# Kernel tuning notes

Measured on AMD Instinct MI355X. Metric: run time of the kernel, lower is better.

The kernel has to match this reference:

```python
import jax, jax.numpy as jnp
import numpy as np

NUM_SEM, MAXPP, FS, FG, H, ITERS, ETN, GROUPS = 24, 10, 128, 128, 128, 2, 4, 16
N_NODES, N_EDGES = 20000, 320000


def _leaky(x):
    return jax.nn.leaky_relu(x, 0.01)


def _lin_init(k, din, dout):
    kw, kb = jax.random.split(k)
    lim = 1.0 / np.sqrt(din)
    w = jax.random.uniform(kw, (dout, din), jnp.float32, -lim, lim)
    b = jax.random.uniform(kb, (dout,), jnp.float32, -lim, lim)
    return w, b


def setup_inputs() -> dict:
    key = jax.random.key(0)
    ks = jax.random.split(key, 16)
    inp = {}
    inp["child_feats"] = jax.random.normal(ks[0], (1, N_NODES, NUM_SEM + MAXPP + FS), jnp.float32)
    inp["child_geo_feats"] = jax.random.normal(ks[1], (1, N_NODES, FG), jnp.float32)
    inp["child_exists"] = jnp.ones((1, N_NODES, 1), jnp.float32)
    inp["edge_type_onehot"] = jax.random.uniform(ks[2], (1, N_EDGES, ETN), jnp.float32)
    inp["edge_indices"] = jax.random.randint(ks[3], (1, N_EDGES, 2), 0, N_NODES)
    inp["child_op_w"], inp["child_op_b"] = _lin_init(ks[4], NUM_SEM + MAXPP + FS, H)
    inp["second_w"], inp["second_b"] = _lin_init(ks[5], H * (ITERS + 1), FS)
    ew, eb = zip(*[_lin_init(ks[6 + i], 2 * H + ETN, H) for i in range(ITERS)])
    inp["edge_w"] = jnp.stack(ew)
    inp["edge_b"] = jnp.stack(eb)
    inp["child_geo_w"], inp["child_geo_b"] = _lin_init(ks[10], FG, H)
    inp["second_geo_w"], inp["second_geo_b"] = _lin_init(ks[11], H, FG)
    inp["gn_w"] = jnp.ones((FG,), jnp.float32)
    inp["gn_b"] = jnp.zeros((FG,), jnp.float32)
    inp["skip_w"], inp["skip_b"] = _lin_init(ks[12], FG, FG)
    return inp


def _group_norm(x, w, b, groups=GROUPS, eps=1e-5):
    # x: [B, C]  (torch GroupNorm on 2D input)
    B, C = x.shape
    xg = x.reshape(B, groups, C // groups)
    mu = xg.mean(axis=-1, keepdims=True)
    var = xg.var(axis=-1, keepdims=True)
    xn = ((xg - mu) * jax.lax.rsqrt(var + eps)).reshape(B, C)
    return xn * w + b


def reference(child_feats, child_geo_feats, child_exists, edge_type_onehot, edge_indices,
              child_op_w, child_op_b, second_w, second_b, edge_w, edge_b,
              child_geo_w, child_geo_b, second_geo_w, second_geo_b, gn_w, gn_b, skip_w, skip_b):
    B, N, _ = child_feats.shape
    # struct branch
    cf = (child_feats @ child_op_w.T + child_op_b) * child_exists  # [B,N,H]
    iter_parent_feats = [cf.max(axis=1)]                           # symmetric_type='max'
    idx_from = edge_indices[0, :, 0]
    idx_to = edge_indices[0, :, 1]
    ef = edge_type_onehot[0]                                       # [E,ETN]
    for i in range(ITERS):
        # gather endpoints, concat edge type, edge-MLP + leaky relu
        msg = jnp.concatenate([cf[0, idx_from], cf[0, idx_to], ef], axis=1)  # [E,2H+ETN]
        msg = _leaky(msg @ edge_w[i].T + edge_b[i])                          # [E,H]
        # scatter_max into zero-initialized node slots (matches torch_scatter with out=zeros)
        cf = jnp.zeros((N, H), msg.dtype).at[idx_from].max(msg)[None]        # [1,N,H]
        iter_parent_feats.append(cf.max(axis=1))
    parent_feat = _leaky(jnp.concatenate(iter_parent_feats, axis=1) @ second_w.T + second_b)
    # geo branch
    skip = (child_geo_feats @ skip_w.T + skip_b) * child_exists    # [B,N,FG]
    cg = (child_geo_feats @ child_geo_w.T + child_geo_b) * child_exists  # [B,N,H]
    pg = _leaky(cg.max(axis=1))
    sg = _leaky(skip.max(axis=1))
    parent_geo_feat = _leaky(sg + _group_norm(pg @ second_geo_w.T + second_geo_b, gn_w, gn_b))
    return parent_feat, parent_geo_feat
```

## Files before the change

### kernel.cpp

```cpp
#include <hip/hip_runtime.h>

#define N_NODES 20000
#define N_EDGES 320000
#define HD 128
#define FIN 162
#define KE 260
#define KPAD 288
#define KOP 192
#define OSTR 200
#define GSTR 136
#define TSTR 136
#define YSTR 136
#define MAXD 64

typedef unsigned short u16;
typedef __attribute__((ext_vector_type(8))) short bf16x8;
typedef __attribute__((ext_vector_type(4))) float f32x4;

__device__ __forceinline__ float leaky(float x){ return fmaxf(x, 0.01f*x); }
__device__ __forceinline__ unsigned fmap(float f){
    unsigned u = __float_as_uint(f);
    return (u & 0x80000000u) ? ~u : (u | 0x80000000u);
}
__device__ __forceinline__ float funmap(unsigned u){
    return __uint_as_float((u & 0x80000000u) ? (u & 0x7fffffffu) : ~u);
}
__device__ __forceinline__ unsigned umax_(unsigned a, unsigned b){ return a > b ? a : b; }
__device__ __forceinline__ u16 f2bf(float x){
    unsigned b = __float_as_uint(x);
    return (u16)((b + 0x7fffu + ((b >> 16) & 1u)) >> 16);
}
__device__ __forceinline__ float bf2f(u16 u){
    return __uint_as_float(((unsigned)u) << 16);
}
__device__ __forceinline__ unsigned cvt_pk_bf16(float lo, float hi){
    unsigned r;
    asm("v_cvt_pk_bf16_f32 %0, %1, %2" : "=v"(r) : "v"(lo), "v"(hi));
    return r;
}

#define PB_W 16
#define PB_F 960
#define PB_G 640
#define PB_H 320
#define PREP_GRID (PB_W + PB_F + PB_G + PB_H)

__global__ __launch_bounds__(256) void prep(
    const float* __restrict__ edge_w, const float* __restrict__ edge_bias,
    u16* __restrict__ Wb,
    const float* __restrict__ op_w,   u16* __restrict__ Wop,
    const float* __restrict__ geo_w,  u16* __restrict__ Wgeo,
    const float* __restrict__ skip_w, u16* __restrict__ Wskip,
    const float* __restrict__ feats,  u16* __restrict__ featsb,
    const float* __restrict__ geof,   u16* __restrict__ geob,
    const int* __restrict__ eidx, const float* __restrict__ ef,
    int* __restrict__ cursor, int4* __restrict__ edat_p)
{
    const int b = blockIdx.x, t = threadIdx.x;
    if (b < PB_W) {
        for (int idx = b * 256 + t; idx < 16384; idx += PB_W * 256) {
            union { u16 us[8]; uint4 v; } pk;
            if (idx < 9216) {
                int layer = idx / 4608, rem = idx - layer * 4608;
                int h = rem / 36, j = rem - h * 36;
                const float* src = edge_w + (size_t)layer * 128 * KE + h * KE;
                #pragma unroll
                for (int kk = 0; kk < 8; ++kk) {
                    int k = j * 8 + kk;
                    pk.us[kk] = (k < KE) ? f2bf(src[k])
                              : (k == 260) ? f2bf(edge_bias[layer * 128 + h])
                              : (u16)0;
                }
                ((uint4*)Wb)[(size_t)layer * 128 * 36 + h * 36 + j] = pk.v;
            } else if (idx < 12288) {
                int rem = idx - 9216;
                int h = rem / 24, j = rem - h * 24;
                const float* src = op_w + h * FIN;
                #pragma unroll
                for (int kk = 0; kk < 8; ++kk) {
                    int k = j * 8 + kk;
                    pk.us[kk] = (k < FIN) ? f2bf(src[k]) : (u16)0;
                }
                ((uint4*)Wop)[h * 24 + j] = pk.v;
            } else {
                int rem = idx - 12288;
                int which = rem >> 11;
                int r2 = rem & 2047;
                const float4* src = (const float4*)((which ? skip_w : geo_w)) + r2 * 2;
                float4 a = src[0], c = src[1];
                pk.us[0]=f2bf(a.x); pk.us[1]=f2bf(a.y); pk.us[2]=f2bf(a.z); pk.us[3]=f2bf(a.w);
                pk.us[4]=f2bf(c.x); pk.us[5]=f2bf(c.y); pk.us[6]=f2bf(c.z); pk.us[7]=f2bf(c.w);
                ((uint4*)(which ? Wskip : Wgeo))[r2] = pk.v;
            }
        }
    } else if (b < PB_W + PB_F) {
        for (int f = (b - PB_W) * 256 + t; f < N_NODES * 24; f += PB_F * 256) {
            int n = f / 24, j = f - n * 24;
            union { u16 us[8]; uint4 v; } pk;
            if (j < 20) {
                const float2* src = (const float2*)(feats + (size_t)n * FIN + j * 8);
                float2 p0 = src[0], p1 = src[1], p2 = src[2], p3 = src[3];
                pk.us[0]=f2bf(p0.x); pk.us[1]=f2bf(p0.y); pk.us[2]=f2bf(p1.x); pk.us[3]=f2bf(p1.y);
                pk.us[4]=f2bf(p2.x); pk.us[5]=f2bf(p2.y); pk.us[6]=f2bf(p3.x); pk.us[7]=f2bf(p3.y);
            } else if (j == 20) {
                float2 p = *(const float2*)(feats + (size_t)n * FIN + 160);
                pk.us[0]=f2bf(p.x); pk.us[1]=f2bf(p.y);
                pk.us[2]=pk.us[3]=pk.us[4]=pk.us[5]=pk.us[6]=pk.us[7]=0;
            } else {
                #pragma unroll
                for (int kk = 0; kk < 8; ++kk) pk.us[kk] = 0;
            }
            ((uint4*)featsb)[(size_t)n * 24 + j] = pk.v;
        }
    } else if (b < PB_W + PB_F + PB_G) {
        for (int g = (b - PB_W - PB_F) * 256 + t; g < N_NODES * 16; g += PB_G * 256) {
            const float4* s = (const float4*)geof + (size_t)g * 2;
            float4 a = s[0], c = s[1];
            union { u16 us[8]; uint4 v; } pk;
            pk.us[0]=f2bf(a.x); pk.us[1]=f2bf(a.y); pk.us[2]=f2bf(a.z); pk.us[3]=f2bf(a.w);
            pk.us[4]=f2bf(c.x); pk.us[5]=f2bf(c.y); pk.us[6]=f2bf(c.z); pk.us[7]=f2bf(c.w);
            ((uint4*)geob)[g] = pk.v;
        }
    } else {
        for (int e = (b - PB_W - PB_F - PB_G) * 256 + t; e < N_EDGES; e += PB_H * 256) {
            int2 p = ((const int2*)eidx)[e];
            int slot = atomicAdd(&cursor[p.x], 1);
            if (slot < MAXD) {
                float4 e4 = ((const float4*)ef)[e];
                edat_p[(size_t)p.x * MAXD + slot] = make_int4(p.y,
                    (int)((unsigned)f2bf(e4.x) | ((unsigned)f2bf(e4.y) << 16)),
                    (int)((unsigned)f2bf(e4.z) | ((unsigned)f2bf(e4.w) << 16)), 0);
            }
        }
    }
}

__global__ __launch_bounds__(256) void mid(
    const u16* __restrict__ featsb, const u16* __restrict__ geob,
    const float* __restrict__ exists,
    const u16* __restrict__ Wop, const float* __restrict__ op_b,
    const u16* __restrict__ Wgeo, const float* __restrict__ geo_b,
    const u16* __restrict__ Wskip, const float* __restrict__ skip_b,
    u16* __restrict__ cf_a,
    unsigned* __restrict__ ipf0_m, unsigned* __restrict__ pg_m,
    unsigned* __restrict__ sg_m)
{
    __shared__ __align__(16) u16 smem[128 * OSTR];
    __shared__ float ex_s[128];
    __shared__ unsigned colmax_s[128];

    const int b = blockIdx.x, t = threadIdx.x;
    const int mode = (b < 157) ? 0 : (b < 314) ? 1 : 2;
    const int bx = b - (mode == 0 ? 0 : mode == 1 ? 157 : 314);
    const int base = bx * 128;
    const int wave = t >> 6, l = t & 63;
    const int quad = l >> 4, lc = l & 15;
    const int R0 = (wave >> 1) * 64;
    const int C0 = (wave & 1) * 64;

    const u16* W = (mode == 0) ? Wop : (mode == 1) ? Wgeo : Wskip;
    const float* bias = (mode == 0) ? op_b : (mode == 1) ? geo_b : skip_b;
    unsigned* accout = (mode == 0) ? ipf0_m : (mode == 1) ? pg_m : sg_m;
    const int KW = (mode == 0) ? KOP : HD;
    const int SW = (mode == 0) ? OSTR : GSTR;
    const int NCH = (mode == 0) ? 6 : 4;
    const u16* A = (mode == 0) ? featsb : geob;

    {
        const int r = t >> 1, half = t & 1;
        const int nu4 = KW / 16;
        const uint4* src = (const uint4*)(W + (size_t)r * KW) + half * nu4;
        uint4* dst = (uint4*)(smem + r * SW) + half * nu4;
        for (int i = 0; i < nu4; ++i) dst[i] = src[i];
    }
    if (t < 128) {
        int n = base + t; if (n >= N_NODES) n = N_NODES - 1;
        ex_s[t] = exists[n];
        colmax_s[t] = 0u;
    }
    __syncthreads();

    f32x4 acc[4][4];
    #pragma unroll
    for (int i = 0; i < 4; ++i)
        #pragma unroll
        for (int j = 0; j < 4; ++j) acc[i][j] = (f32x4){0.f, 0.f, 0.f, 0.f};

    int nd[4];
    #pragma unroll
    for (int ti = 0; ti < 4; ++ti) {
        int n = base + R0 + ti * 16 + lc;
        nd[ti] = (n < N_NODES) ? n : N_NODES - 1;
    }

    for (int c = 0; c < NCH; ++c) {
        bf16x8 af[4], bfr[4];
        #pragma unroll
        for (int ti = 0; ti < 4; ++ti)
            af[ti] = *(const bf16x8*)(A + (size_t)nd[ti] * KW + c * 32 + quad * 8);
        #pragma unroll
        for (int tj = 0; tj < 4; ++tj)
            bfr[tj] = *(const bf16x8*)(smem + (C0 + tj * 16 + lc) * SW + c * 32 + quad * 8);
        #pragma unroll
        for (int ti = 0; ti < 4; ++ti)
            #pragma unroll
            for (int tj = 0; tj < 4; ++tj)
                acc[ti][tj] = __builtin_amdgcn_mfma_f32_16x16x32_bf16(
                    af[ti], bfr[tj], acc[ti][tj], 0, 0, 0);
    }

    #pragma unroll
    for (int tj = 0; tj < 4; ++tj) {
        const int col = C0 + tj * 16 + lc;
        const float bc = bias[col];
        unsigned mx = 0u;
        #pragma unroll
        for (int ti = 0; ti < 4; ++ti) {
            #pragma unroll
            for (int r = 0; r < 4; ++r) {
                int row = R0 + ti * 16 + quad * 4 + r;
                float x = (acc[ti][tj][r] + bc) * ex_s[row];
                acc[ti][tj][r] = x;
                mx = umax_(mx, fmap(x));
            }
        }
        atomicMax(&colmax_s[col], mx);
    }
    __syncthreads();
    if (t < 128) atomicMax(&accout[t], colmax_s[t]);

    if (mode == 0) {
        #pragma unroll
        for (int ti = 0; ti < 4; ++ti)
            #pragma unroll
            for (int tj = 0; tj < 4; ++tj) {
                const int col = C0 + tj * 16 + lc;
                #pragma unroll
                for (int r = 0; r < 4; ++r)
                    smem[(R0 + ti * 16 + quad * 4 + r) * TSTR + col] = f2bf(acc[ti][tj][r]);
            }
        __syncthreads();
        #pragma unroll
        for (int i = 0; i < 8; ++i) {
            int idx = t + i * 256;
            int row = idx >> 4, c16 = idx & 15;
            int n = base + row;
            if (n < N_NODES) {
                uint4 v = *(const uint4*)(smem + row * TSTR + c16 * 8);
                *(uint4*)(cf_a + (size_t)n * HD + c16 * 8) = v;
            }
        }
    }
}

__global__ __launch_bounds__(512) void ygemm(
    const u16* __restrict__ cf,
    const u16* __restrict__ Wb_l,
    const float* __restrict__ eb,
    float* __restrict__ Yf,
    u16* __restrict__ Ytb)
{
    __shared__ __align__(16) u16 smem[256 * YSTR];
    const int t = threadIdx.x;
    const int base = blockIdx.x * 64;
    const int wave = t >> 6, l = t & 63;
    const int quad = l >> 4, lc = l & 15;
    const int C0 = wave * 32;

    for (int idx = t; idx < 4096; idx += 512) {
        int r = idx >> 4, j = idx & 15;
        const uint4* src = (const uint4*)(Wb_l +
            (size_t)((r < 128) ? r * KPAD : (r - 128) * KPAD + 128));
        ((uint4*)(smem + r * YSTR))[j] = src[j];
    }
    __syncthreads();

    f32x4 acc[4][2];
    #pragma unroll
    for (int i = 0; i < 4; ++i)
        #pragma unroll
        for (int j = 0; j < 2; ++j) acc[i][j] = (f32x4){0.f, 0.f, 0.f, 0.f};

    int nd[4];
    #pragma unroll
    for (int ti = 0; ti < 4; ++ti) {
        int n = base + ti * 16 + lc;
        nd[ti] = (n < N_NODES) ? n : N_NODES - 1;
    }

    #pragma unroll
    for (int c = 0; c < 4; ++c) {
        bf16x8 af[4], bfr[2];
        #pragma unroll
        for (int ti = 0; ti < 4; ++ti)
            af[ti] = *(const bf16x8*)(cf + (size_t)nd[ti] * HD + c * 32 + quad * 8);
        #pragma unroll
        for (int tj = 0; tj < 2; ++tj)
            bfr[tj] = *(const bf16x8*)(smem + (C0 + tj * 16 + lc) * YSTR + c * 32 + quad * 8);
        #pragma unroll
        for (int ti = 0; ti < 4; ++ti)
            #pragma unroll
            for (int tj = 0; tj < 2; ++tj)
                acc[ti][tj] = __builtin_amdgcn_mfma_f32_16x16x32_bf16(
                    af[ti], bfr[tj], acc[ti][tj], 0, 0, 0);
    }

    #pragma unroll
    for (int tj = 0; tj < 2; ++tj) {
        const int col = C0 + tj * 16 + lc;
        const float bc = (col >= 128) ? eb[col & 127] : 0.f;
        #pragma unroll
        for (int ti = 0; ti < 4; ++ti) {
            #pragma unroll
            for (int r = 0; r < 4; ++r) {
                int row = base + ti * 16 + quad * 4 + r;
                if (row < N_NODES) {
                    if (col < 128)
                        Yf[(size_t)row * HD + col] = acc[ti][tj][r];
                    else
                        Ytb[(size_t)row * HD + (col & 127)] = f2bf(acc[ti][tj][r] + bc);
                }
            }
        }
    }
}

#define EP_BLOCKS 1024
#define EP_WAVES  (EP_BLOCKS * 8)

template<int WRITE_CF>
__global__ __launch_bounds__(512) void epass(
    const float* __restrict__ Yf,
    const u16* __restrict__ Ytb,
    const int4* __restrict__ edat,
    const u16* __restrict__ Wb_l,
    const int* __restrict__ cnt,
    u16* __restrict__ cf_bb,
    int* __restrict__ ipf_out)
{
    __shared__ int ipf_s[128];
    const int t = threadIdx.x;
    const int l = t & 63;
    const int gw = __builtin_amdgcn_readfirstlane(blockIdx.x * 8 + (t >> 6));
    if (t < 128) ipf_s[t] = 0;

    const uint2 wua = *(const uint2*)(Wb_l + (size_t)(2 * l) * KPAD + 256);
    const uint2 wub = *(const uint2*)(Wb_l + (size_t)(2 * l + 1) * KPAD + 256);
    const float wa0 = bf2f((u16)wua.x), wa1 = bf2f((u16)(wua.x >> 16));
    const float wa2 = bf2f((u16)wua.y), wa3 = bf2f((u16)(wua.y >> 16));
    const float wb0 = bf2f((u16)wub.x), wb1 = bf2f((u16)(wub.x >> 16));
    const float wb2 = bf2f((u16)wub.y), wb3 = bf2f((u16)(wub.y >> 16));

    float ipf0 = 0.f, ipf1 = 0.f;

#define EPROC(D, YT) do { \
    float _e0 = bf2f((u16)(unsigned)(D).y), _e1 = bf2f((u16)(((unsigned)(D).y) >> 16)); \
    float _e2 = bf2f((u16)(unsigned)(D).z), _e3 = bf2f((u16)(((unsigned)(D).z) >> 16)); \
    float _ya = bf2f((u16)(YT)), _yb = bf2f((u16)((YT) >> 16)); \
    float _s0 = yfx + _ya; \
    _s0 = fmaf(_e0, wa0, _s0); _s0 = fmaf(_e1, wa1, _s0); \
    _s0 = fmaf(_e2, wa2, _s0); _s0 = fmaf(_e3, wa3, _s0); \
    _s0 = leaky(_s0); mx0 = fmaxf(mx0, _s0); \
    float _s1 = yfy + _yb; \
    _s1 = fmaf(_e0, wb0, _s1); _s1 = fmaf(_e1, wb1, _s1); \
    _s1 = fmaf(_e2, wb2, _s1); _s1 = fmaf(_e3, wb3, _s1); \
    _s1 = leaky(_s1); mx1 = fmaxf(mx1, _s1); \
} while (0)

#define YLOAD(D) (*(const unsigned*)(Ytb + (size_t)(D).x * HD + 2 * l))

    for (int n = gw; n < N_NODES; n += EP_WAVES) {
        const int c0 = cnt[n];
        const int c = (c0 < MAXD) ? c0 : MAXD;
        const int o = n * MAXD;
        const float2 yf = *(const float2*)(Yf + (size_t)n * HD + 2 * l);
        const float yfx = yf.x, yfy = yf.y;
        float mx0 = 0.f, mx1 = 0.f;

        int i = 0;
        for (; i + 8 <= c; i += 8) {
            const int e = o + i;
            int4 d0 = edat[e],     d1 = edat[e + 1], d2 = edat[e + 2], d3 = edat[e + 3];
            int4 d4 = edat[e + 4], d5 = edat[e + 5], d6 = edat[e + 6], d7 = edat[e + 7];
            unsigned y0 = YLOAD(d0), y1 = YLOAD(d1), y2 = YLOAD(d2), y3 = YLOAD(d3);
            unsigned y4 = YLOAD(d4), y5 = YLOAD(d5), y6 = YLOAD(d6), y7 = YLOAD(d7);
            EPROC(d0, y0); EPROC(d1, y1); EPROC(d2, y2); EPROC(d3, y3);
            EPROC(d4, y4); EPROC(d5, y5); EPROC(d6, y6); EPROC(d7, y7);
        }
        for (; i + 2 <= c; i += 2) {
            const int e = o + i;
            int4 d0 = edat[e], d1 = edat[e + 1];
            unsigned y0 = YLOAD(d0), y1 = YLOAD(d1);
            EPROC(d0, y0); EPROC(d1, y1);
        }
        if (i < c) {
            int4 d0 = edat[o + i];
            unsigned y0 = YLOAD(d0);
            EPROC(d0, y0);
        }

        if (WRITE_CF) {
            unsigned pk = cvt_pk_bf16(mx0, mx1);
            *(unsigned*)(cf_bb + (size_t)n * HD + 2 * l) = pk;
        }
        ipf0 = fmaxf(ipf0, mx0);
        ipf1 = fmaxf(ipf1, mx1);
    }
#undef EPROC
#undef YLOAD

    __syncthreads();
    atomicMax(&ipf_s[2 * l],     __float_as_int(ipf0));
    atomicMax(&ipf_s[2 * l + 1], __float_as_int(ipf1));
    __syncthreads();
    if (t < 128) atomicMax(&ipf_out[t], ipf_s[t]);
}

__global__ __launch_bounds__(128) void heads(
    const unsigned* __restrict__ ipf0_m,
    const float* __restrict__ ipf1, const float* __restrict__ ipf2,
    const float* __restrict__ secW, const float* __restrict__ secB,
    const unsigned* __restrict__ pg_m, const unsigned* __restrict__ sg_m,
    const float* __restrict__ geoW, const float* __restrict__ geoB,
    const float* __restrict__ gnw, const float* __restrict__ gnb,
    float* __restrict__ out)
{
    const int t = threadIdx.x;
    if (blockIdx.x == 0) {
        __shared__ float s[384];
        s[t]       = funmap(ipf0_m[t]);
        s[128 + t] = ipf1[t];
        s[256 + t] = ipf2[t];
        __syncthreads();
        float acc = secB[t];
        #pragma unroll 4
        for (int k = 0; k < 384; ++k) acc = fmaf(s[k], secW[t*384 + k], acc);
        out[t] = leaky(acc);
    } else {
        __shared__ float pg[128];
        __shared__ float tt[128];
        pg[t] = leaky(funmap(pg_m[t]));
        float sg = leaky(funmap(sg_m[t]));
        __syncthreads();
        float acc = geoB[t];
        #pragma unroll 4
        for (int k = 0; k < 128; ++k) acc = fmaf(pg[k], geoW[t*128 + k], acc);
        tt[t] = acc;
        __syncthreads();
        const int g = (t >> 3) << 3;
        float mu = 0.f, m2 = 0.f;
        #pragma unroll
        for (int q = 0; q < 8; ++q) { float x = tt[g + q]; mu += x; m2 += x*x; }
        mu *= 0.125f;
        m2 = m2 * 0.125f - mu * mu;
        float xn = (acc - mu) * rsqrtf(m2 + 1e-5f);
        out[128 + t] = leaky(sg + xn * gnw[t] + gnb[t]);
    }
}

extern "C" void kernel_launch(void* const* d_in, const int* in_sizes, int n_in,
                              void* d_out, int out_size, void* d_ws, size_t ws_size,
                              hipStream_t stream)
{
    const float* child_feats  = (const float*)d_in[0];
    const float* child_geo    = (const float*)d_in[1];
    const float* child_exists = (const float*)d_in[2];
    const float* etoh         = (const float*)d_in[3];
    const int*   eidx         = (const int*)  d_in[4];
    const float* op_w   = (const float*)d_in[5];
    const float* op_b   = (const float*)d_in[6];
    const float* sec_w  = (const float*)d_in[7];
    const float* sec_b  = (const float*)d_in[8];
    const float* edge_w = (const float*)d_in[9];
    const float* edge_b = (const float*)d_in[10];
    const float* geo_w  = (const float*)d_in[11];
    const float* geo_b  = (const float*)d_in[12];
    const float* sgeo_w = (const float*)d_in[13];
    const float* sgeo_b = (const float*)d_in[14];
    const float* gn_w   = (const float*)d_in[15];
    const float* gn_b   = (const float*)d_in[16];
    const float* skip_w = (const float*)d_in[17];
    const float* skip_b = (const float*)d_in[18];
    float* out = (float*)d_out;

    char* ws = (char*)d_ws;
    size_t off = 0;
    u16*   cf_a   = (u16*)(ws + off);   off += (size_t)N_NODES*HD*2;
    char*  uni    = ws + off;           off += (size_t)N_NODES*HD*6;
    u16*   featsb = (u16*)uni;
    u16*   geob   = (u16*)(uni + (size_t)N_NODES*KOP*2);
    float* Yf     = (float*)uni;
    u16*   Ytb    = (u16*)(uni + (size_t)N_NODES*HD*4);
    u16*   Wb     = (u16*)(ws + off);   off += (size_t)2*128*KPAD*2;
    u16*   Wop    = (u16*)(ws + off);   off += (size_t)128*KOP*2;
    u16*   Wgeo   = (u16*)(ws + off);   off += (size_t)128*128*2;
    u16*   Wskip  = (u16*)(ws + off);   off += (size_t)128*128*2;
    int4*  edat_p = (int4*)(ws + off);  off += (size_t)N_NODES*MAXD*16;
    u16*   cf_bb  = (u16*)(ws + off);   off += (size_t)N_NODES*HD*2;
    char*  zero0  = ws + off;
    unsigned* ipf0_m = (unsigned*)(ws + off); off += 128*4;
    float*    ipf1   = (float*)(ws + off);    off += 128*4;
    float*    ipf2   = (float*)(ws + off);    off += 128*4;
    unsigned* pg_m   = (unsigned*)(ws + off); off += 128*4;
    unsigned* sg_m   = (unsigned*)(ws + off); off += 128*4;
    int*      cursor = (int*)(ws + off);      off += (size_t)N_NODES*4;
    size_t zero_bytes = (size_t)(ws + off - zero0);

    hipMemsetAsync(zero0, 0, zero_bytes, stream);

    prep<<<PREP_GRID, 256, 0, stream>>>(
        edge_w, edge_b, Wb, op_w, Wop, geo_w, Wgeo, skip_w, Wskip,
        child_feats, featsb, child_geo, geob, eidx, etoh, cursor, edat_p);

    mid<<<471, 256, 0, stream>>>(
        featsb, geob, child_exists, Wop, op_b, Wgeo, geo_b, Wskip, skip_b,
        cf_a, ipf0_m, pg_m, sg_m);

    ygemm<<<313, 512, 0, stream>>>(cf_a, Wb, edge_b, Yf, Ytb);
    epass<1><<<EP_BLOCKS, 512, 0, stream>>>(
        Yf, Ytb, edat_p, Wb, cursor, cf_bb, (int*)ipf1);

    ygemm<<<313, 512, 0, stream>>>(cf_bb, Wb + 128*KPAD, edge_b + 128, Yf, Ytb);
    epass<0><<<EP_BLOCKS, 512, 0, stream>>>(
        Yf, Ytb, edat_p, Wb + 128*KPAD, cursor, nullptr, (int*)ipf2);

    heads<<<2, 128, 0, stream>>>(ipf0_m, ipf1, ipf2, sec_w, sec_b,
                                 pg_m, sg_m, sgeo_w, sgeo_b, gn_w, gn_b, out);
}
```

Measured before the change: 248.2 us.

## Fuse heads into last edge pass and store Y as interleaved bf16

The separate heads kernel is removed. Its work now runs in the last block of the second edge pass, chosen by an atomic completion counter after a threadfence. The Y buffers are merged into one bf16 array with 256 columns per node, so the self term is stored in bf16 instead of fp32. This saves one kernel launch and some memory traffic, at the cost of lower precision on the self term and a serial tail inside the final block.

```diff
diff --git a/kernel.cpp b/kernel.cpp
--- a/kernel.cpp
+++ b/kernel.cpp
@@ -257,8 +257,7 @@
     const u16* __restrict__ cf,
     const u16* __restrict__ Wb_l,
     const float* __restrict__ eb,
-    float* __restrict__ Yf,
-    u16* __restrict__ Ytb)
+    u16* __restrict__ Yb)
 {
     __shared__ __align__(16) u16 smem[256 * YSTR];
     const int t = threadIdx.x;
@@ -314,12 +313,8 @@
             #pragma unroll
             for (int r = 0; r < 4; ++r) {
                 int row = base + ti * 16 + quad * 4 + r;
-                if (row < N_NODES) {
-                    if (col < 128)
-                        Yf[(size_t)row * HD + col] = acc[ti][tj][r];
-                    else
-                        Ytb[(size_t)row * HD + (col & 127)] = f2bf(acc[ti][tj][r] + bc);
-                }
+                if (row < N_NODES)
+                    Yb[(size_t)row * 256 + col] = f2bf(acc[ti][tj][r] + bc);
             }
         }
     }
@@ -328,15 +323,21 @@
 #define EP_BLOCKS 1024
 #define EP_WAVES  (EP_BLOCKS * 8)
 
-template<int WRITE_CF>
+template<int WRITE_CF, int DO_HEADS>
 __global__ __launch_bounds__(512) void epass(
-    const float* __restrict__ Yf,
-    const u16* __restrict__ Ytb,
+    const u16* __restrict__ Yb,
     const int4* __restrict__ edat,
     const u16* __restrict__ Wb_l,
     const int* __restrict__ cnt,
     u16* __restrict__ cf_bb,
-    int* __restrict__ ipf_out)
+    int* __restrict__ ipf_out,
+    int* __restrict__ done,
+    const unsigned* __restrict__ ipf0_m, const float* __restrict__ ipf1,
+    const float* __restrict__ secW, const float* __restrict__ secB,
+    const unsigned* __restrict__ pg_m, const unsigned* __restrict__ sg_m,
+    const float* __restrict__ geoW, const float* __restrict__ geoB,
+    const float* __restrict__ gnw, const float* __restrict__ gnb,
+    float* __restrict__ out)
 {
     __shared__ int ipf_s[128];
     const int t = threadIdx.x;
@@ -351,7 +352,7 @@
     const float wb0 = bf2f((u16)wub.x), wb1 = bf2f((u16)(wub.x >> 16));
     const float wb2 = bf2f((u16)wub.y), wb3 = bf2f((u16)(wub.y >> 16));
 
-    float ipf0 = 0.f, ipf1 = 0.f;
+    float ipf0 = 0.f, ipf1v = 0.f;
 
 #define EPROC(D, YT) do { \
     float _e0 = bf2f((u16)(unsigned)(D).y), _e1 = bf2f((u16)(((unsigned)(D).y) >> 16)); \
@@ -367,14 +368,14 @@
     _s1 = leaky(_s1); mx1 = fmaxf(mx1, _s1); \
 } while (0)
 
-#define YLOAD(D) (*(const unsigned*)(Ytb + (size_t)(D).x * HD + 2 * l))
+#define YLOAD(D) (*(const unsigned*)(Yb + (size_t)(D).x * 256 + 128 + 2 * l))
 
     for (int n = gw; n < N_NODES; n += EP_WAVES) {
         const int c0 = cnt[n];
         const int c = (c0 < MAXD) ? c0 : MAXD;
         const int o = n * MAXD;
-        const float2 yf = *(const float2*)(Yf + (size_t)n * HD + 2 * l);
-        const float yfx = yf.x, yfy = yf.y;
+        const unsigned yfp = *(const unsigned*)(Yb + (size_t)n * 256 + 2 * l);
+        const float yfx = bf2f((u16)yfp), yfy = bf2f((u16)(yfp >> 16));
         float mx0 = 0.f, mx1 = 0.f;
 
         int i = 0;
@@ -404,57 +405,63 @@
             *(unsigned*)(cf_bb + (size_t)n * HD + 2 * l) = pk;
         }
         ipf0 = fmaxf(ipf0, mx0);
-        ipf1 = fmaxf(ipf1, mx1);
+        ipf1v = fmaxf(ipf1v, mx1);
     }
 #undef EPROC
 #undef YLOAD
 
     __syncthreads();
     atomicMax(&ipf_s[2 * l],     __float_as_int(ipf0));
-    atomicMax(&ipf_s[2 * l + 1], __float_as_int(ipf1));
+    atomicMax(&ipf_s[2 * l + 1], __float_as_int(ipf1v));
     __syncthreads();
     if (t < 128) atomicMax(&ipf_out[t], ipf_s[t]);
-}
-
-__global__ __launch_bounds__(128) void heads(
-    const unsigned* __restrict__ ipf0_m,
-    const float* __restrict__ ipf1, const float* __restrict__ ipf2,
-    const float* __restrict__ secW, const float* __restrict__ secB,
-    const unsigned* __restrict__ pg_m, const unsigned* __restrict__ sg_m,
-    const float* __restrict__ geoW, const float* __restrict__ geoB,
-    const float* __restrict__ gnw, const float* __restrict__ gnb,
-    float* __restrict__ out)
-{
-    const int t = threadIdx.x;
-    if (blockIdx.x == 0) {
-        __shared__ float s[384];
-        s[t]       = funmap(ipf0_m[t]);
-        s[128 + t] = ipf1[t];
-        s[256 + t] = ipf2[t];
-        __syncthreads();
-        float acc = secB[t];
-        #pragma unroll 4
-        for (int k = 0; k < 384; ++k) acc = fmaf(s[k], secW[t*384 + k], acc);
-        out[t] = leaky(acc);
-    } else {
+
+    if (DO_HEADS) {
+        __shared__ int lastflag;
+        __shared__ float hs[384];
         __shared__ float pg[128];
         __shared__ float tt[128];
-        pg[t] = leaky(funmap(pg_m[t]));
-        float sg = leaky(funmap(sg_m[t]));
+        __threadfence();
         __syncthreads();
-        float acc = geoB[t];
-        #pragma unroll 4
-        for (int k = 0; k < 128; ++k) acc = fmaf(pg[k], geoW[t*128 + k], acc);
-        tt[t] = acc;
+        if (t == 0) lastflag = (atomicAdd(done, 1) == EP_BLOCKS - 1);
         __syncthreads();
-        const int g = (t >> 3) << 3;
-        float mu = 0.f, m2 = 0.f;
-        #pragma unroll
-        for (int q = 0; q < 8; ++q) { float x = tt[g + q]; mu += x; m2 += x*x; }
-        mu *= 0.125f;
-        m2 = m2 * 0.125f - mu * mu;
-        float xn = (acc - mu) * rsqrtf(m2 + 1e-5f);
-        out[128 + t] = leaky(sg + xn * gnw[t] + gnb[t]);
+        if (lastflag) {
+            float sg = 0.f, acc = 0.f;
+            if (t < 128) {
+                hs[t]       = funmap(ipf0_m[t]);
+                hs[128 + t] = ipf1[t];
+                hs[256 + t] = __int_as_float(atomicOr(&ipf_out[t], 0));
+            } else if (t < 256) {
+                const int q = t - 128;
+                pg[q] = leaky(funmap(pg_m[q]));
+                sg    = leaky(funmap(sg_m[q]));
+            }
+            __syncthreads();
+            if (t < 128) {
+                acc = secB[t];
+                #pragma unroll 4
+                for (int k = 0; k < 384; ++k) acc = fmaf(hs[k], secW[t*384 + k], acc);
+                out[t] = leaky(acc);
+            } else if (t < 256) {
+                const int q = t - 128;
+                acc = geoB[q];
+                #pragma unroll 4
+                for (int k = 0; k < 128; ++k) acc = fmaf(pg[k], geoW[q*128 + k], acc);
+                tt[q] = acc;
+            }
+            __syncthreads();
+            if (t >= 128 && t < 256) {
+                const int q = t - 128;
+                const int g = (q >> 3) << 3;
+                float mu = 0.f, m2 = 0.f;
+                #pragma unroll
+                for (int qq = 0; qq < 8; ++qq) { float x = tt[g + qq]; mu += x; m2 += x*x; }
+                mu *= 0.125f;
+                m2 = m2 * 0.125f - mu * mu;
+                float xn = (acc - mu) * rsqrtf(m2 + 1e-5f);
+                out[128 + q] = leaky(sg + xn * gnw[q] + gnb[q]);
+            }
+        }
     }
 }
 
@@ -486,11 +493,10 @@
     char* ws = (char*)d_ws;
     size_t off = 0;
     u16*   cf_a   = (u16*)(ws + off);   off += (size_t)N_NODES*HD*2;
-    char*  uni    = ws + off;           off += (size_t)N_NODES*HD*6;
+    char*  uni    = ws + off;           off += (size_t)N_NODES*(KOP+HD)*2;
     u16*   featsb = (u16*)uni;
     u16*   geob   = (u16*)(uni + (size_t)N_NODES*KOP*2);
-    float* Yf     = (float*)uni;
-    u16*   Ytb    = (u16*)(uni + (size_t)N_NODES*HD*4);
+    u16*   Yb     = (u16*)uni;
     u16*   Wb     = (u16*)(ws + off);   off += (size_t)2*128*KPAD*2;
     u16*   Wop    = (u16*)(ws + off);   off += (size_t)128*KOP*2;
     u16*   Wgeo   = (u16*)(ws + off);   off += (size_t)128*128*2;
@@ -503,6 +509,7 @@
     float*    ipf2   = (float*)(ws + off);    off += 128*4;
     unsigned* pg_m   = (unsigned*)(ws + off); off += 128*4;
     unsigned* sg_m   = (unsigned*)(ws + off); off += 128*4;
+    int*      done   = (int*)(ws + off);      off += 16;
     int*      cursor = (int*)(ws + off);      off += (size_t)N_NODES*4;
     size_t zero_bytes = (size_t)(ws + off - zero0);
 
@@ -516,14 +523,13 @@
         featsb, geob, child_exists, Wop, op_b, Wgeo, geo_b, Wskip, skip_b,
         cf_a, ipf0_m, pg_m, sg_m);
 
-    ygemm<<<313, 512, 0, stream>>>(cf_a, Wb, edge_b, Yf, Ytb);
-    epass<1><<<EP_BLOCKS, 512, 0, stream>>>(
-        Yf, Ytb, edat_p, Wb, cursor, cf_bb, (int*)ipf1);
-
-    ygemm<<<313, 512, 0, stream>>>(cf_bb, Wb + 128*KPAD, edge_b + 128, Yf, Ytb);
-    epass<0><<<EP_BLOCKS, 512, 0, stream>>>(
-        Yf, Ytb, edat_p, Wb + 128*KPAD, cursor, nullptr, (int*)ipf2);
-
-    heads<<<2, 128, 0, stream>>>(ipf0_m, ipf1, ipf2, sec_w, sec_b,
-                                 pg_m, sg_m, sgeo_w, sgeo_b, gn_w, gn_b, out);
-}
+    ygemm<<<313, 512, 0, stream>>>(cf_a, Wb, edge_b, Yb);
+    epass<1, 0><<<EP_BLOCKS, 512, 0, stream>>>(
+        Yb, edat_p, Wb, cursor, cf_bb, (int*)ipf1, done,
+        ipf0_m, ipf1, sec_w, sec_b, pg_m, sg_m, sgeo_w, sgeo_b, gn_w, gn_b, out);
+
+    ygemm<<<313, 512, 0, stream>>>(cf_bb, Wb + 128*KPAD, edge_b + 128, Yb);
+    epass<0, 1><<<EP_BLOCKS, 512, 0, stream>>>(
+        Yb, edat_p, Wb + 128*KPAD, cursor, nullptr, (int*)ipf2, done,
+        ipf0_m, ipf1, sec_w, sec_b, pg_m, sg_m, sgeo_w, sgeo_b, gn_w, gn_b, out);
+}
```

After: 370.4 us. 1.49x slower.
